# Kernel tuning notes

Hardware: AMD Instinct MI355X
Metric: run time of the kernel (lower is better)

## Reference

```python
import jax, jax.numpy as jnp
import numpy as np

WS = 11
SIGMA = 1.5
CH = 3
C1 = (0.01 * 255.0) ** 2  # 6.5025
C2 = (0.03 * 255.0) ** 2  # 58.5225


def _gauss_window():
    # 1D Gaussian -> outer product -> depthwise kernel [C, 1, ws, ws] (OIHW)
    coords = jnp.arange(WS, dtype=jnp.float32) - WS // 2
    g = jnp.exp(-coords ** 2 / (2.0 * SIGMA ** 2))
    g = g / g.sum()
    w2d = g[:, None] * g[None, :]
    return jnp.tile(w2d[None, None], (CH, 1, 1, 1))


def _dwconv(x, win):
    pad = WS // 2
    return jax.lax.conv_general_dilated(
        x, win, window_strides=(1, 1), padding=[(pad, pad), (pad, pad)],
        feature_group_count=CH,
        dimension_numbers=('NCHW', 'OIHW', 'NCHW'))


def setup_inputs() -> dict:
    key = jax.random.key(0)
    k1, k2 = jax.random.split(key)
    shape = (32, 3, 512, 512)
    img_gen = jax.random.uniform(k1, shape, jnp.float32, -1.0, 1.0)
    img_ref = jax.random.uniform(k2, shape, jnp.float32, -1.0, 1.0)
    return {"img_gen": img_gen, "img_ref": img_ref}


def reference(img_gen, img_ref):
    gen = (img_gen + 1.0) * 0.5
    ref = (img_ref + 1.0) * 0.5
    win = _gauss_window()

    mu1 = _dwconv(gen, win)
    mu2 = _dwconv(ref, win)
    mu1_sq = mu1 * mu1
    mu2_sq = mu2 * mu2
    mu1_mu2 = mu1 * mu2
    sigma1_sq = _dwconv(gen * gen, win) - mu1_sq
    sigma2_sq = _dwconv(ref * ref, win) - mu2_sq
    sigma12 = _dwconv(gen * ref, win) - mu1_mu2

    ssim_map = ((2.0 * mu1_mu2 + C1) * (2.0 * sigma12 + C2)) / (
        (mu1_sq + mu2_sq + C1) * (sigma1_sq + sigma2_sq + C2))
    return 1.0 - ssim_map.mean()
```

## Files before the change

kernel.cpp:

```cpp
#include <hip/hip_runtime.h>

typedef float v2f __attribute__((ext_vector_type(2)));

#define TY 8
#define WIN 18
#define CST 33
#define RST (5 * CST)
#define SWV (WIN * RST)
#define IMW 512
#define IMH 512
#define NPLANES 96
#define NSX 16
#define NSEG 2
#define NCH 32
#define NWAVES (NSX * NSEG * NPLANES)
#define NBLOCKS (NWAVES / 4)

#define GW0 0.00102838f
#define GW1 0.00759877f
#define GW2 0.03600077f
#define GW3 0.10936069f
#define GW4 0.21300553f
#define GW5 0.26601172f

__device__ __forceinline__ void pkfma(v2f& acc, v2f a, v2f b) {
  asm("v_pk_fma_f32 %0, %1, %2, %0" : "+v"(acc) : "v"(a), "v"(b));
}
__device__ __forceinline__ v2f pkmul(v2f a, v2f b) {
  v2f d;
  asm("v_pk_mul_f32 %0, %1, %2" : "=v"(d) : "v"(a), "v"(b));
  return d;
}

__device__ __forceinline__ void hblur(
    const float* __restrict__ gp, const float* __restrict__ rp,
    float* __restrict__ sq, int x0, bool fast, int nrows, int gy0,
    int slot0, int hr, int xs) {
  if (hr >= nrows) return;
  const float GW[11] = {GW0, GW1, GW2, GW3, GW4, GW5,
                        GW4, GW3, GW2, GW1, GW0};
  const int gy = gy0 + hr;
  int slot = slot0 + hr;
  if (slot >= WIN) slot -= WIN;
  const int xbase = x0 + xs - 8;
  const float* grow = gp + (size_t)gy * IMW;
  const float* rrow = rp + (size_t)gy * IMW;

  v2f P[14];
#define PUT1(idx, gc, rc)                                                    \
  do {                                                                       \
    if ((idx) >= 3 && (idx) <= 16)                                           \
      P[(idx) - 3] = (v2f){fmaf(0.5f, (gc), 0.5f), fmaf(0.5f, (rc), 0.5f)};  \
  } while (0)
  if (fast) {
#pragma unroll
    for (int k = 0; k < 5; ++k) {
      const float4 g4 = *(const float4*)(grow + xbase + 4 * k);
      const float4 r4 = *(const float4*)(rrow + xbase + 4 * k);
      PUT1(4 * k + 0, g4.x, r4.x);
      PUT1(4 * k + 1, g4.y, r4.y);
      PUT1(4 * k + 2, g4.z, r4.z);
      PUT1(4 * k + 3, g4.w, r4.w);
    }
  } else {
    const bool rowok = (gy >= 0) & (gy < IMH);
#pragma unroll
    for (int k = 0; k < 5; ++k) {
      const int c = xbase + 4 * k;
      const bool ok = rowok && (c >= 0) && (c < IMW);
      float4 g4 = make_float4(-1.f, -1.f, -1.f, -1.f);
      float4 r4 = g4;
      if (ok) {
        g4 = *(const float4*)(grow + c);
        r4 = *(const float4*)(rrow + c);
      }
      PUT1(4 * k + 0, g4.x, r4.x);
      PUT1(4 * k + 1, g4.y, r4.y);
      PUT1(4 * k + 2, g4.z, r4.z);
      PUT1(4 * k + 3, g4.w, r4.w);
    }
  }
#undef PUT1

  v2f accP[4], accQ[4];
  float accS[4];
#pragma unroll
  for (int o = 0; o < 4; ++o) {
    accP[o] = (v2f){0.f, 0.f};
    accQ[o] = (v2f){0.f, 0.f};
    accS[o] = 0.f;
  }

#pragma unroll
  for (int p = 0; p < 14; ++p) {
    const v2f pv = P[p];
    const v2f qv = pkmul(pv, pv);
    const float sv = pv.x * pv.y;
    const int olo = (p - 10 < 0) ? 0 : p - 10;
    const int ohi = (p < 3) ? p : 3;
#pragma unroll
    for (int o = olo; o <= ohi; ++o) {
      const float wt = GW[p - o];
      const v2f wv = (v2f){wt, wt};
      pkfma(accP[o], wv, pv);
      pkfma(accQ[o], wv, qv);
      accS[o] = fmaf(wt, sv, accS[o]);
    }
  }

  float* dst = sq + slot * RST + xs;
#pragma unroll
  for (int o = 0; o < 4; ++o) dst[0 * CST + o] = accP[o].x;
#pragma unroll
  for (int o = 0; o < 4; ++o) dst[1 * CST + o] = accP[o].y;
#pragma unroll
  for (int o = 0; o < 4; ++o) dst[2 * CST + o] = accQ[o].x;
#pragma unroll
  for (int o = 0; o < 4; ++o) dst[3 * CST + o] = accQ[o].y;
#pragma unroll
  for (int o = 0; o < 4; ++o) dst[4 * CST + o] = accS[o];
}

__device__ __forceinline__ float ssim_px(v2f mu, v2f ee, float e12) {
  const float C1 = 6.5025f, C2 = 58.5225f;
  const float mu1 = mu.x, mu2 = mu.y, e1 = ee.x, e2 = ee.y;
  const float m12 = mu1 * mu2;
  const float m1s = mu1 * mu1;
  const float m2s = mu2 * mu2;
  const float num = (2.f * m12 + C1) * (2.f * (e12 - m12) + C2);
  const float den = (m1s + m2s + C1) * ((e1 - m1s) + (e2 - m2s) + C2);
  return __fdividef(num, den);
}

__device__ __forceinline__ float vchunk(
    const float* __restrict__ sq, int wb, int col, int r0) {
  const float GW[11] = {GW0, GW1, GW2, GW3, GW4, GW5,
                        GW4, GW3, GW2, GW1, GW0};
  v2f mu[4], ee[4];
  float e12[4];
#pragma unroll
  for (int o = 0; o < 4; ++o) {
    mu[o] = (v2f){0.f, 0.f};
    ee[o] = (v2f){0.f, 0.f};
    e12[o] = 0.f;
  }
#pragma unroll
  for (int i = 0; i < 14; ++i) {
    int slot = wb + r0 + i;
    if (slot >= WIN) slot -= WIN;
    const float* rowp = sq + slot * RST + col;
    const v2f hp = (v2f){rowp[0 * CST], rowp[1 * CST]};
    const v2f hq = (v2f){rowp[2 * CST], rowp[3 * CST]};
    const float hsv = rowp[4 * CST];
    const int olo = (i - 10 < 0) ? 0 : i - 10;
    const int ohi = (i < 3) ? i : 3;
#pragma unroll
    for (int o = olo; o <= ohi; ++o) {
      const float wt = GW[i - o];
      const v2f wv = (v2f){wt, wt};
      pkfma(mu[o], wv, hp);
      pkfma(ee[o], wv, hq);
      e12[o] = fmaf(wt, hsv, e12[o]);
    }
  }
  return (ssim_px(mu[0], ee[0], e12[0]) + ssim_px(mu[1], ee[1], e12[1])) +
         (ssim_px(mu[2], ee[2], e12[2]) + ssim_px(mu[3], ee[3], e12[3]));
}

__global__ __launch_bounds__(256, 3) void ssim_main(
    const float* __restrict__ gen, const float* __restrict__ ref,
    double* __restrict__ partial) {
  __shared__ float ring[4][SWV];

  const int tid = threadIdx.x;
  const int wv = tid >> 6;
  const int lane = tid & 63;
  const int wid = (blockIdx.x << 2) | wv;
  const int plane = wid >> 5;
  const int rem = wid & 31;
  const int sx = rem & 15;
  const int seg = rem >> 4;
  const int x0 = sx * 32;
  const int Y0 = seg * 256;
  const float* gp = gen + (size_t)plane * (IMW * IMH);
  const float* rp = ref + (size_t)plane * (IMW * IMH);
  float* const sq = &ring[wv][0];
  const bool fx = (sx >= 1) & (sx <= NSX - 2);

  const int hr = lane >> 3;
  const int xs = (lane & 7) * 4;
  const int col = lane & 31;
  const int r0 = (lane >> 5) * 4;

  hblur(gp, rp, sq, x0, fx & (seg > 0), 8, Y0 - 5, 0, hr, xs);
  hblur(gp, rp, sq, x0, fx, 8, Y0 + 3, 8, hr, xs);
  hblur(gp, rp, sq, x0, fx, 2, Y0 + 11, 16, hr, xs);

  double acc = 0.0;
  int wb = 0;
#pragma unroll 1
  for (int c = 0; c < NCH; ++c) {
    acc += (double)vchunk(sq, wb, col, r0);
    if (c < NCH - 1) {
      const int gy0 = Y0 + 13 + TY * c;
      hblur(gp, rp, sq, x0, fx && (gy0 + TY <= IMH), TY, gy0, wb, hr, xs);
    }
    wb += TY;
    if (wb >= WIN) wb -= WIN;
  }

#pragma unroll
  for (int off = 32; off > 0; off >>= 1) acc += __shfl_down(acc, off, 64);
  if (lane == 0) partial[wid] = acc;
}

__global__ void ssim_reduce(const double* __restrict__ partial,
                            float* __restrict__ out) {
  const int tid = threadIdx.x;
  double s = 0.0;
  for (int i = tid; i < NWAVES; i += 256) s += partial[i];
#pragma unroll
  for (int off = 32; off > 0; off >>= 1) s += __shfl_down(s, off, 64);
  __shared__ double sd[4];
  if ((tid & 63) == 0) sd[tid >> 6] = s;
  __syncthreads();
  if (tid == 0) {
    const double npix = (double)NPLANES * (double)IMW * (double)IMH;
    out[0] = (float)(1.0 - (sd[0] + sd[1] + sd[2] + sd[3]) / npix);
  }
}

extern "C" void kernel_launch(void* const* d_in, const int* in_sizes, int n_in,
                              void* d_out, int out_size, void* d_ws, size_t ws_size,
                              hipStream_t stream) {
  (void)in_sizes; (void)n_in; (void)out_size; (void)ws_size;
  const float* gen = (const float*)d_in[0];
  const float* ref = (const float*)d_in[1];
  double* partial = (double*)d_ws;
  ssim_main<<<NBLOCKS, 256, 0, stream>>>(gen, ref, partial);
  ssim_reduce<<<1, 256, 0, stream>>>(partial, (float*)d_out);
}
```

Before: 299.1 us.

## Software-pipeline global row loads one chunk ahead of horizontal blur

Splits the horizontal blur into a load phase and a compute-and-store phase, and prefetches the next chunk's global rows into registers while the current chunk's vertical blur and horizontal store run. The aim is to hide global memory latency behind LDS and ALU work inside each wave's loop. The cost is about 40 extra live VGPRs for the prefetched float4s, which could hurt occupancy under launch_bounds(256,3) or cause spills.

```diff
diff --git a/kernel.cpp b/kernel.cpp
--- a/kernel.cpp
+++ b/kernel.cpp
@@ -32,35 +32,23 @@
   return d;
 }
 
-__device__ __forceinline__ void hblur(
+struct Raw {
+  float4 g[5];
+  float4 r[5];
+};
+
+__device__ __forceinline__ void hload(
     const float* __restrict__ gp, const float* __restrict__ rp,
-    float* __restrict__ sq, int x0, bool fast, int nrows, int gy0,
-    int slot0, int hr, int xs) {
-  if (hr >= nrows) return;
-  const float GW[11] = {GW0, GW1, GW2, GW3, GW4, GW5,
-                        GW4, GW3, GW2, GW1, GW0};
+    int x0, bool fast, int gy0, int hr, int xs, Raw& L) {
   const int gy = gy0 + hr;
-  int slot = slot0 + hr;
-  if (slot >= WIN) slot -= WIN;
   const int xbase = x0 + xs - 8;
   const float* grow = gp + (size_t)gy * IMW;
   const float* rrow = rp + (size_t)gy * IMW;
-
-  v2f P[14];
-#define PUT1(idx, gc, rc)                                                    \
-  do {                                                                       \
-    if ((idx) >= 3 && (idx) <= 16)                                           \
-      P[(idx) - 3] = (v2f){fmaf(0.5f, (gc), 0.5f), fmaf(0.5f, (rc), 0.5f)};  \
-  } while (0)
   if (fast) {
 #pragma unroll
     for (int k = 0; k < 5; ++k) {
-      const float4 g4 = *(const float4*)(grow + xbase + 4 * k);
-      const float4 r4 = *(const float4*)(rrow + xbase + 4 * k);
-      PUT1(4 * k + 0, g4.x, r4.x);
-      PUT1(4 * k + 1, g4.y, r4.y);
-      PUT1(4 * k + 2, g4.z, r4.z);
-      PUT1(4 * k + 3, g4.w, r4.w);
+      L.g[k] = *(const float4*)(grow + xbase + 4 * k);
+      L.r[k] = *(const float4*)(rrow + xbase + 4 * k);
     }
   } else {
     const bool rowok = (gy >= 0) & (gy < IMH);
@@ -74,11 +62,33 @@
         g4 = *(const float4*)(grow + c);
         r4 = *(const float4*)(rrow + c);
       }
-      PUT1(4 * k + 0, g4.x, r4.x);
-      PUT1(4 * k + 1, g4.y, r4.y);
-      PUT1(4 * k + 2, g4.z, r4.z);
-      PUT1(4 * k + 3, g4.w, r4.w);
-    }
+      L.g[k] = g4;
+      L.r[k] = r4;
+    }
+  }
+}
+
+__device__ __forceinline__ void hstore(
+    const Raw& L, float* __restrict__ sq, int slot0, int hr, int xs) {
+  const float GW[11] = {GW0, GW1, GW2, GW3, GW4, GW5,
+                        GW4, GW3, GW2, GW1, GW0};
+  int slot = slot0 + hr;
+  if (slot >= WIN) slot -= WIN;
+
+  v2f P[14];
+#define PUT1(idx, gc, rc)                                                    \
+  do {                                                                       \
+    if ((idx) >= 3 && (idx) <= 16)                                           \
+      P[(idx) - 3] = (v2f){fmaf(0.5f, (gc), 0.5f), fmaf(0.5f, (rc), 0.5f)};  \
+  } while (0)
+#pragma unroll
+  for (int k = 0; k < 5; ++k) {
+    const float4 g4 = L.g[k];
+    const float4 r4 = L.r[k];
+    PUT1(4 * k + 0, g4.x, r4.x);
+    PUT1(4 * k + 1, g4.y, r4.y);
+    PUT1(4 * k + 2, g4.z, r4.z);
+    PUT1(4 * k + 3, g4.w, r4.w);
   }
 #undef PUT1
 
@@ -119,6 +129,16 @@
   for (int o = 0; o < 4; ++o) dst[3 * CST + o] = accQ[o].y;
 #pragma unroll
   for (int o = 0; o < 4; ++o) dst[4 * CST + o] = accS[o];
+}
+
+__device__ __forceinline__ void hblur(
+    const float* __restrict__ gp, const float* __restrict__ rp,
+    float* __restrict__ sq, int x0, bool fast, int nrows, int gy0,
+    int slot0, int hr, int xs) {
+  if (hr >= nrows) return;
+  Raw t;
+  hload(gp, rp, x0, fast, gy0, hr, xs, t);
+  hstore(t, sq, slot0, hr, xs);
 }
 
 __device__ __forceinline__ float ssim_px(v2f mu, v2f ee, float e12) {
@@ -196,14 +216,20 @@
   hblur(gp, rp, sq, x0, fx, 8, Y0 + 3, 8, hr, xs);
   hblur(gp, rp, sq, x0, fx, 2, Y0 + 11, 16, hr, xs);
 
+  Raw L;
+  hload(gp, rp, x0, fx, Y0 + 13, hr, xs, L);
+
   double acc = 0.0;
   int wb = 0;
 #pragma unroll 1
   for (int c = 0; c < NCH; ++c) {
     acc += (double)vchunk(sq, wb, col, r0);
     if (c < NCH - 1) {
-      const int gy0 = Y0 + 13 + TY * c;
-      hblur(gp, rp, sq, x0, fx && (gy0 + TY <= IMH), TY, gy0, wb, hr, xs);
+      hstore(L, sq, wb, hr, xs);
+      if (c < NCH - 2) {
+        const int gy0 = Y0 + 21 + TY * c;
+        hload(gp, rp, x0, fx && (gy0 + TY <= IMH), gy0, hr, xs, L);
+      }
     }
     wb += TY;
     if (wb >= WIN) wb -= WIN;
```

Result: slower. 377.8 us (+26.3%).
